# Kernel optimization log

Measured on AMD Instinct MI355X. Metric: run time of the kernel, lower is better.

## Reference

```python
import jax, jax.numpy as jnp
import numpy as np

B, S, D, H, TILES = 4, 1024, 1024, 16, 8
DFF = 4 * D
EPS = 1e-5

def setup_inputs() -> dict:
    key = jax.random.key(0)
    ks = jax.random.split(key, 8)
    p = lambda k, shape: jax.random.normal(k, shape, dtype=jnp.float32) * 0.02
    return dict(
        x=jax.random.normal(ks[0], (B, S, D), dtype=jnp.float32),
        ln1_g=jnp.ones((D,), jnp.float32), ln1_b=jnp.zeros((D,), jnp.float32),
        qkv_w=p(ks[1], (3 * D, D)), qkv_b=jnp.zeros((3 * D,), jnp.float32),
        out_w=p(ks[2], (D, D)), out_b=jnp.zeros((D,), jnp.float32),
        ln2_g=jnp.ones((D,), jnp.float32), ln2_b=jnp.zeros((D,), jnp.float32),
        gate_w=p(ks[3], (TILES, D)), gate_b=jnp.zeros((TILES,), jnp.float32),
        up_W=p(ks[4], (TILES, D, DFF)), up_b=jnp.zeros((TILES, DFF), jnp.float32),
        down_W=p(ks[5], (TILES, DFF, D)), down_b=jnp.zeros((TILES, D), jnp.float32),
    )

def _layernorm(x, g, b):
    m = jnp.mean(x, axis=-1, keepdims=True)
    v = jnp.var(x, axis=-1, keepdims=True)
    return (x - m) * jax.lax.rsqrt(v + EPS) * g + b

def _mha(x, qkv_w, qkv_b, out_w, out_b):
    b, s, d = x.shape
    hd = d // H
    qkv = x @ qkv_w.T + qkv_b                       # [b, s, 3d]
    q, k, v = jnp.split(qkv, 3, axis=-1)
    q = q.reshape(b, s, H, hd)
    k = k.reshape(b, s, H, hd)
    v = v.reshape(b, s, H, hd)
    scores = jnp.einsum('bqhd,bkhd->bhqk', q, k) / jnp.sqrt(jnp.float32(hd))
    p = jax.nn.softmax(scores, axis=-1)
    o = jnp.einsum('bhqk,bkhd->bqhd', p, v).reshape(b, s, d)
    return o @ out_w.T + out_b

def _gated_ffn(t, gate_w, gate_b, up_W, up_b, down_W, down_b):
    # t: [N, D] tokens. Top-1 hard gate with straight-through estimator.
    logits = t @ gate_w.T + gate_b                  # [N, TILES]
    hard = jax.nn.one_hot(jnp.argmax(logits, axis=-1), TILES, dtype=logits.dtype)
    gate = hard + logits - jax.lax.stop_gradient(logits)
    # TriXLinear: one-hot-selected per-tile GEMM, expressed as gated contraction.
    h = jax.nn.relu(jnp.einsum('nt,ni,tio->no', gate, t, up_W) + gate @ up_b)
    out = jnp.einsum('nt,nh,tho->no', gate, h, down_W) + gate @ down_b
    return out, gate

def reference(x, ln1_g, ln1_b, qkv_w, qkv_b, out_w, out_b, ln2_g, ln2_b,
              gate_w, gate_b, up_W, up_b, down_W, down_b):
    n1 = _layernorm(x, ln1_g, ln1_b)
    x = x + _mha(n1, qkv_w, qkv_b, out_w, out_b)
    n2 = _layernorm(x, ln2_g, ln2_b)
    t = n2.reshape(-1, D)
    ffn, gate = _gated_ffn(t, gate_w, gate_b, up_W, up_b, down_W, down_b)
    out = x + ffn.reshape(x.shape)
    return (out, gate.reshape(B, S, TILES))
```

## Files before the change

### kernel.cpp

```cpp
#include <hip/hip_runtime.h>

typedef __attribute__((ext_vector_type(8))) short short8;
typedef __attribute__((ext_vector_type(4))) float f32x4;

__device__ __forceinline__ float bf2f(unsigned short h){
  return __uint_as_float(((unsigned)h) << 16);
}
__device__ __forceinline__ unsigned short f2bf(float f){
  unsigned u = __float_as_uint(f);
  u += 0x7FFFu + ((u >> 16) & 1u);
  return (unsigned short)(u >> 16);
}
__device__ __forceinline__ f32x4 mfma16(short8 a, short8 b, f32x4 c){
  return __builtin_amdgcn_mfma_f32_16x16x32_bf16(a, b, c, 0, 0, 0);
}
__device__ __forceinline__ short8 ld8(const unsigned short* p){
  return *reinterpret_cast<const short8*>(p);
}

__global__ __launch_bounds__(256) void wsplit_k(const float* __restrict__ w,
    unsigned short* __restrict__ hi, unsigned short* __restrict__ lo, int n)
{
  const int i = (blockIdx.x*256 + threadIdx.x)*4;
  if (i >= n) return;
  const float4 v = *(const float4*)(w + i);
  float a[4] = {v.x, v.y, v.z, v.w};
  #pragma unroll
  for (int j=0;j<4;j++){
    unsigned short h = f2bf(a[j]);
    hi[i+j] = h;
    lo[i+j] = f2bf(a[j] - bf2f(h));
  }
}

__global__ __launch_bounds__(256) void wtrans_k(const float* __restrict__ in,
    unsigned short* __restrict__ out, int K, int N)
{
  __shared__ float t[32][33];
  const int z = blockIdx.z;
  const float* inz = in + (long)z*K*N;
  unsigned short* outz = out + (long)z*K*N;
  const int c0 = blockIdx.x*32, r0 = blockIdx.y*32;
  const int tx = threadIdx.x & 31, ty = threadIdx.x >> 5;
  #pragma unroll
  for (int i=0;i<4;i++)
    t[ty+8*i][tx] = inz[(long)(r0+ty+8*i)*N + c0+tx];
  __syncthreads();
  #pragma unroll
  for (int i=0;i<4;i++)
    outz[(long)(c0+ty+8*i)*K + r0+tx] = f2bf(t[tx][ty+8*i]);
}

__global__ __launch_bounds__(256) void ln_k(const float* __restrict__ xin,
    const float* __restrict__ g, const float* __restrict__ bb,
    unsigned short* __restrict__ oh, unsigned short* __restrict__ ol,
    float* __restrict__ ofull)
{
  const int row = blockIdx.x, tid = threadIdx.x;
  const int ln = tid & 63, wv = tid >> 6;
  const float4 f = *(const float4*)(xin + (long)row*1024 + tid*4);
  float v[4] = {f.x, f.y, f.z, f.w};
  float s = v[0]+v[1]+v[2]+v[3];
  float q = v[0]*v[0]+v[1]*v[1]+v[2]*v[2]+v[3]*v[3];
  #pragma unroll
  for (int m=1;m<64;m<<=1){ s += __shfl_xor(s,m,64); q += __shfl_xor(q,m,64); }
  __shared__ float rs[4], rq[4];
  if (ln==0){ rs[wv]=s; rq[wv]=q; }
  __syncthreads();
  s = rs[0]+rs[1]+rs[2]+rs[3];
  q = rq[0]+rq[1]+rq[2]+rq[3];
  const float mean = s * (1.f/1024.f);
  const float var  = q * (1.f/1024.f) - mean*mean;
  const float rinv = 1.f / sqrtf(var + 1e-5f);
  #pragma unroll
  for (int j=0;j<4;j++){
    const int c = tid*4 + j;
    const float nv = (v[j]-mean)*rinv*g[c] + bb[c];
    const unsigned short hi = f2bf(nv);
    oh[(long)row*1024 + c] = hi;
    if (ol)    ol[(long)row*1024 + c] = f2bf(nv - bf2f(hi));
    if (ofull) ofull[(long)row*1024 + c] = nv;
  }
}

template<int AMODE, int EPI, bool GATHER>
__global__ __launch_bounds__(256) void gemm_k(
    const unsigned short* __restrict__ Ah, const unsigned short* __restrict__ Al, int lda,
    const unsigned short* __restrict__ Bh, const unsigned short* __restrict__ Bl,
    int ldb, int K, int N,
    const float* __restrict__ bias,
    const float* __restrict__ resx, const float* __restrict__ resx2,
    unsigned short* __restrict__ oh, unsigned short* __restrict__ ol,
    float* __restrict__ of,
    unsigned short* __restrict__ vt1, unsigned short* __restrict__ vt2,
    const int* __restrict__ idx, const int* __restrict__ cnt, int Mtot)
{
  constexpr int NB = (AMODE==1) ? 2 : 1;
  constexpr int LDW = 40;
  __shared__ unsigned short As[NB][128*LDW];
  __shared__ unsigned short Bs[NB][128*LDW];
  __shared__ long arowS[128];
  __shared__ int  atokS[128];

  const int tid = threadIdx.x, wv = tid>>6, ln = tid&63, l16 = ln&15, qd = ln>>4;
  int M = Mtot;
  int z, mblk, nblk;
  if constexpr (GATHER){
    z = blockIdx.y; mblk = blockIdx.z; nblk = blockIdx.x;
  } else {
    z = blockIdx.z; mblk = blockIdx.x; nblk = blockIdx.y;
  }
  const int* idz = nullptr;
  if constexpr (GATHER){
    M = cnt[z];
    if (mblk*128 >= M) return;
    idz = idx + z*4096;
  }
  const int m0 = mblk*128, n0 = nblk*128;
  const unsigned short* Bz = Bh + (GATHER ? (long)z*(long)K*(long)N : 0);

  if (tid < 128){
    const int mi = m0 + tid;
    const int mc = mi < M ? mi : (M-1);
    const int tok = GATHER ? idz[mc] : mc;
    arowS[tid] = (long)tok * lda;
    atokS[tid] = tok;
  }
  __syncthreads();

  f32x4 acc[4][4];
  #pragma unroll
  for (int i=0;i<4;i++)
    #pragma unroll
    for (int w=0;w<4;w++) acc[i][w] = f32x4{0.f,0.f,0.f,0.f};

  const int mloc = (wv&1)*64, nloc = (wv>>1)*64;
  const int srow0 = tid>>2, scoff = (tid&3)*8;

  for (int k0=0; k0<K; k0+=32){
    #pragma unroll
    for (int i=0;i<2;i++){
      const int row = srow0 + i*64;
      const long ao = arowS[row] + k0 + scoff;
      const long bo = (long)(n0+row)*ldb + k0 + scoff;
      *(short8*)&As[0][row*LDW + scoff] = ld8(Ah + ao);
      *(short8*)&Bs[0][row*LDW + scoff] = ld8(Bz + bo);
      if constexpr (AMODE==1){
        *(short8*)&As[1][row*LDW + scoff] = ld8(Al + ao);
        *(short8*)&Bs[1][row*LDW + scoff] = ld8(Bl + bo);
      }
    }
    __syncthreads();
    short8 a0[4], a1[4], b0[4], b1[4];
    #pragma unroll
    for (int i=0;i<4;i++){
      a0[i] = *(const short8*)&As[0][(mloc+i*16+l16)*LDW + qd*8];
      if constexpr (AMODE==1) a1[i] = *(const short8*)&As[1][(mloc+i*16+l16)*LDW + qd*8];
    }
    #pragma unroll
    for (int w=0;w<4;w++){
      b0[w] = *(const short8*)&Bs[0][(nloc+w*16+l16)*LDW + qd*8];
      if constexpr (AMODE==1) b1[w] = *(const short8*)&Bs[1][(nloc+w*16+l16)*LDW + qd*8];
    }
    #pragma unroll
    for (int i=0;i<4;i++)
      #pragma unroll
      for (int w=0;w<4;w++){
        acc[i][w] = mfma16(a0[i], b0[w], acc[i][w]);
        if constexpr (AMODE==1){
          acc[i][w] = mfma16(a0[i], b1[w], acc[i][w]);
          acc[i][w] = mfma16(a1[i], b0[w], acc[i][w]);
        }
      }
    __syncthreads();
  }
  #pragma unroll
  for (int i=0;i<4;i++){
    #pragma unroll
    for (int w=0;w<4;w++){
      const int col = n0 + nloc + w*16 + l16;
      const float bv = bias[(GATHER ? z*N : 0) + col];
      #pragma unroll
      for (int r=0;r<4;r++){
        const int lrow = mloc + i*16 + qd*4 + r;
        if (m0 + lrow >= M) continue;
        const int tok = atokS[lrow];
        float v = acc[i][w][r] + bv;
        if constexpr (EPI==0){
          const unsigned short hi = f2bf(v);
          const unsigned short lo = f2bf(v - bf2f(hi));
          const long o = (long)tok*3072 + col;
          oh[o] = hi; ol[o] = lo;
          if (col >= 2048){
            const int c = col - 2048;
            const int hh = c >> 6, d = c & 63;
            const int b_ = tok >> 10, ss = tok & 1023;
            const long vo = ((long)((b_*16 + hh)*64 + d))*1024 + ss;
            vt1[vo] = hi; vt2[vo] = lo;
          }
        } else if constexpr (EPI==1){
          v += resx[(long)tok*1024 + col];
          of[(long)tok*1024 + col] = v;
        } else if constexpr (EPI==2){
          v = fmaxf(v, 0.f);
          oh[(long)tok*4096 + col] = f2bf(v);
        } else {
          v += resx2[(long)tok*1024 + col];
          of[(long)tok*1024 + col] = v;
        }
      }
    }
  }
}

__global__ __launch_bounds__(64) void attn_k(
    unsigned short* __restrict__ qkh, unsigned short* __restrict__ qkl,
    const unsigned short* __restrict__ vth, const unsigned short* __restrict__ vtl)
{
  __shared__ float Ps[16][34];
  const int ln = threadIdx.x, l16 = ln&15, qd = ln>>4;
  const int qt = blockIdx.x, h = blockIdx.y, b = blockIdx.z;
  const long qrow = (long)(b*1024 + qt*16 + l16);
  const unsigned short* qp  = qkh + qrow*3072 + h*64 + qd*8;
  const unsigned short* qpl = qkl + qrow*3072 + h*64 + qd*8;
  short8 qh[2], ql[2];
  qh[0] = ld8(qp);  qh[1] = ld8(qp+32);
  ql[0] = ld8(qpl); ql[1] = ld8(qpl+32);
  f32x4 O[4];
  #pragma unroll
  for (int nt=0;nt<4;nt++) O[nt] = f32x4{0.f,0.f,0.f,0.f};
  float mrow[4] = {-3e38f,-3e38f,-3e38f,-3e38f};
  float lrow[4] = {0.f,0.f,0.f,0.f};
  const long vbase = (long)((b*16+h)*64);

  for (int kt=0; kt<32; kt++){
    const int ks0 = kt*32;
    short8 kfh[2][2], kfl[2][2];
    #pragma unroll
    for (int nt2=0;nt2<2;nt2++){
      const long krow = (long)(b*1024 + ks0 + nt2*16 + l16);
      const unsigned short* kp  = qkh + krow*3072 + 1024 + h*64 + qd*8;
      const unsigned short* kpl = qkl + krow*3072 + 1024 + h*64 + qd*8;
      kfh[nt2][0] = ld8(kp);  kfh[nt2][1] = ld8(kp+32);
      kfl[nt2][0] = ld8(kpl); kfl[nt2][1] = ld8(kpl+32);
    }
    f32x4 S0 = f32x4{0.f,0.f,0.f,0.f}, S1 = f32x4{0.f,0.f,0.f,0.f};
    #pragma unroll
    for (int ks=0; ks<2; ks++){
      S0 = mfma16(qh[ks], kfh[0][ks], S0);
      S0 = mfma16(qh[ks], kfl[0][ks], S0);
      S0 = mfma16(ql[ks], kfh[0][ks], S0);
      S1 = mfma16(qh[ks], kfh[1][ks], S1);
      S1 = mfma16(qh[ks], kfl[1][ks], S1);
      S1 = mfma16(ql[ks], kfh[1][ks], S1);
    }
    float p0[4], p1[4], alpha[4];
    #pragma unroll
    for (int r=0;r<4;r++){
      float s0 = S0[r]*0.125f, s1 = S1[r]*0.125f;
      float mx = fmaxf(s0,s1);
      #pragma unroll
      for (int m=1;m<16;m<<=1) mx = fmaxf(mx, __shfl_xor(mx, m, 64));
      float mn = fmaxf(mrow[r], mx);
      float e0 = __expf(s0-mn), e1 = __expf(s1-mn);
      float rsum = e0+e1;
      #pragma unroll
      for (int m=1;m<16;m<<=1) rsum += __shfl_xor(rsum, m, 64);
      float al = __expf(mrow[r]-mn);
      lrow[r] = lrow[r]*al + rsum;
      mrow[r] = mn;
      alpha[r]=al; p0[r]=e0; p1[r]=e1;
    }
    #pragma unroll
    for (int nt=0;nt<4;nt++)
      #pragma unroll
      for (int r=0;r<4;r++) O[nt][r] *= alpha[r];
    #pragma unroll
    for (int r=0;r<4;r++){
      Ps[qd*4+r][l16]      = p0[r];
      Ps[qd*4+r][16+l16]   = p1[r];
    }
    __syncthreads();
    short8 ph, pm, pl;
    #pragma unroll
    for (int j=0;j<8;j++){
      float pv = Ps[l16][qd*8+j];
      unsigned short h1 = f2bf(pv); float r1 = pv - bf2f(h1);
      unsigned short h2 = f2bf(r1); float r2 = r1 - bf2f(h2);
      unsigned short h3 = f2bf(r2);
      ph[j]=(short)h1; pm[j]=(short)h2; pl[j]=(short)h3;
    }
    __syncthreads();
    #pragma unroll
    for (int nt=0;nt<4;nt++){
      const unsigned short* vp  = vth + (vbase + nt*16 + l16)*1024 + ks0 + qd*8;
      const unsigned short* vpl = vtl + (vbase + nt*16 + l16)*1024 + ks0 + qd*8;
      short8 vh = ld8(vp), vl = ld8(vpl);
      O[nt] = mfma16(ph, vh, O[nt]);
      O[nt] = mfma16(ph, vl, O[nt]);
      O[nt] = mfma16(pm, vh, O[nt]);
      O[nt] = mfma16(pl, vh, O[nt]);
    }
  }
  #pragma unroll
  for (int nt=0;nt<4;nt++)
    #pragma unroll
    for (int r=0;r<4;r++){
      float v = O[nt][r] / lrow[r];
      const long row = (long)(b*1024 + qt*16 + qd*4 + r);
      const int col = h*64 + nt*16 + l16;
      const unsigned short hi = f2bf(v);
      qkh[row*3072 + col] = hi;
      qkl[row*3072 + col] = f2bf(v - bf2f(hi));
    }
}

__global__ __launch_bounds__(256) void gate_k(
    const float* __restrict__ n2f, const float* __restrict__ gw, const float* __restrict__ gb,
    float* __restrict__ gout, int* __restrict__ cnt, int* __restrict__ idx)
{
  const int wv = threadIdx.x >> 6, ln = threadIdx.x & 63;
  const int tok = blockIdx.x*4 + wv;
  float xv[16];
  #pragma unroll
  for (int j=0;j<4;j++){
    const float4 f = *(const float4*)(n2f + (long)tok*1024 + ln*16 + j*4);
    xv[j*4]=f.x; xv[j*4+1]=f.y; xv[j*4+2]=f.z; xv[j*4+3]=f.w;
  }
  float lg[8];
  #pragma unroll
  for (int t=0;t<8;t++){
    float s = 0.f;
    #pragma unroll
    for (int j=0;j<4;j++){
      const float4 wf = *(const float4*)(gw + t*1024 + ln*16 + j*4);
      s += xv[j*4]*wf.x + xv[j*4+1]*wf.y + xv[j*4+2]*wf.z + xv[j*4+3]*wf.w;
    }
    #pragma unroll
    for (int m=1;m<64;m<<=1) s += __shfl_xor(s,m,64);
    lg[t] = s + gb[t];
  }
  int best = 0; float bv = lg[0];
  #pragma unroll
  for (int t=1;t<8;t++) if (lg[t] > bv){ bv = lg[t]; best = t; }
  if (ln == 0){
    int pos = atomicAdd(&cnt[best], 1);
    idx[best*4096 + pos] = tok;
  }
  if (ln < 8) gout[(long)tok*8 + ln] = (ln == best) ? 1.0f : 0.0f;
}

extern "C" void kernel_launch(void* const* d_in, const int* in_sizes, int n_in,
                              void* d_out, int out_size, void* d_ws, size_t ws_size,
                              hipStream_t stream)
{
  const float* x     = (const float*)d_in[0];
  const float* ln1g  = (const float*)d_in[1];
  const float* ln1b  = (const float*)d_in[2];
  const float* qkvw  = (const float*)d_in[3];
  const float* qkvb  = (const float*)d_in[4];
  const float* outw  = (const float*)d_in[5];
  const float* outb  = (const float*)d_in[6];
  const float* ln2g  = (const float*)d_in[7];
  const float* ln2b  = (const float*)d_in[8];
  const float* gatew = (const float*)d_in[9];
  const float* gateb = (const float*)d_in[10];
  const float* upW   = (const float*)d_in[11];
  const float* upb   = (const float*)d_in[12];
  const float* dnW   = (const float*)d_in[13];
  const float* dnb   = (const float*)d_in[14];
  float* outp  = (float*)d_out;
  float* gatep = outp + 4194304;

  char* w = (char*)d_ws;
  auto alloc = [&](size_t b){ char* p = w; w += (b + 255) & ~(size_t)255; return p; };
  char* regionA = w;
  unsigned short* n1h  = (unsigned short*)alloc(8388608);
  unsigned short* n1l  = (unsigned short*)alloc(8388608);
  unsigned short* qwh  = (unsigned short*)alloc(6291456);
  unsigned short* qwl  = (unsigned short*)alloc(6291456);
  unsigned short* owh  = (unsigned short*)alloc(2097152);
  unsigned short* owl  = (unsigned short*)alloc(2097152);
  unsigned short* hbuf = (unsigned short*)regionA;
  char* regionB = w;
  unsigned short* qkh  = (unsigned short*)alloc(25165824);
  unsigned short* qkl  = (unsigned short*)alloc(25165824);
  unsigned short* vth  = (unsigned short*)alloc(8388608);
  unsigned short* vtl  = (unsigned short*)alloc(8388608);
  unsigned short* wffn = (unsigned short*)regionB;
  float*          x2   = (float*)alloc(16777216);
  float*          n2f  = (float*)alloc(16777216);
  unsigned short* n2h  = (unsigned short*)alloc(8388608);
  int*            idxb = (int*)alloc(131072);
  int*            cntb = (int*)alloc(256);

  wsplit_k<<<3072,256,0,stream>>>(qkvw, qwh, qwl, 3145728);
  wsplit_k<<<1024,256,0,stream>>>(outw, owh, owl, 1048576);
  ln_k<<<4096,256,0,stream>>>(x, ln1g, ln1b, n1h, n1l, nullptr);
  gemm_k<1,0,false><<<dim3(32,24,1),256,0,stream>>>(
      n1h, n1l, 1024, qwh, qwl, 1024, 1024, 3072, qkvb,
      nullptr, nullptr, qkh, qkl, nullptr, vth, vtl, nullptr, nullptr, 4096);
  attn_k<<<dim3(64,16,4),64,0,stream>>>(qkh, qkl, vth, vtl);
  gemm_k<1,1,false><<<dim3(32,8,1),256,0,stream>>>(
      qkh, qkl, 3072, owh, owl, 1024, 1024, 1024, outb,
      x, nullptr, nullptr, nullptr, x2, nullptr, nullptr, nullptr, nullptr, 4096);
  ln_k<<<4096,256,0,stream>>>(x2, ln2g, ln2b, n2h, nullptr, n2f);
  hipMemsetAsync(cntb, 0, 32, stream);
  gate_k<<<1024,256,0,stream>>>(n2f, gatew, gateb, gatep, cntb, idxb);
  wtrans_k<<<dim3(128,32,8),256,0,stream>>>(upW, wffn, 1024, 4096);
  gemm_k<0,2,true><<<dim3(32,8,32),256,0,stream>>>(
      n2h, nullptr, 1024, wffn, nullptr, 1024, 1024, 4096, upb,
      nullptr, nullptr, hbuf, nullptr, nullptr, nullptr, nullptr, idxb, cntb, 0);
  wtrans_k<<<dim3(32,128,8),256,0,stream>>>(dnW, wffn, 4096, 1024);
  gemm_k<0,3,true><<<dim3(8,8,32),256,0,stream>>>(
      hbuf, nullptr, 4096, wffn, nullptr, 4096, 4096, 1024, dnb,
      nullptr, x2, nullptr, nullptr, outp, nullptr, nullptr, idxb, cntb, 0);
}
```

Before: 1.019 ms.

## Split attention over two key chunks with a separate log-sum-exp merge kernel

The attention kernel now splits the 1024 keys into two halves handled by separate waves, and packs four query-tile waves into each 256-thread block. Each wave writes unnormalised partial outputs plus its running max and sum to a scratch buffer that aliases x2. A new merge kernel combines the two halves with log-sum-exp rescaling and writes the split bf16 hi/lo output. The aim is more waves in flight to hide the latency of the attention loop. The cost is extra partial-result traffic, an additional launch, and scratch writes that exceed x2's allocation and spill into the following buffers.

Result: slower. 1.156 ms (+13.5%).

```diff
diff --git a/kernel.cpp b/kernel.cpp
--- a/kernel.cpp
+++ b/kernel.cpp
@@ -213,13 +213,15 @@
   }
 }
 
-__global__ __launch_bounds__(64) void attn_k(
-    unsigned short* __restrict__ qkh, unsigned short* __restrict__ qkl,
-    const unsigned short* __restrict__ vth, const unsigned short* __restrict__ vtl)
-{
-  __shared__ float Ps[16][34];
-  const int ln = threadIdx.x, l16 = ln&15, qd = ln>>4;
-  const int qt = blockIdx.x, h = blockIdx.y, b = blockIdx.z;
+__global__ __launch_bounds__(256, 8) void attn_k(
+    const unsigned short* __restrict__ qkh, const unsigned short* __restrict__ qkl,
+    const unsigned short* __restrict__ vth, const unsigned short* __restrict__ vtl,
+    float* __restrict__ pbuf)
+{
+  __shared__ float Ps[4][16][34];
+  const int tid = threadIdx.x, wv = tid>>6, ln = tid&63, l16 = ln&15, qd = ln>>4;
+  const int qt = blockIdx.x*4 + wv, h = blockIdx.y;
+  const int c = blockIdx.z >> 2, b = blockIdx.z & 3;
   const long qrow = (long)(b*1024 + qt*16 + l16);
   const unsigned short* qp  = qkh + qrow*3072 + h*64 + qd*8;
   const unsigned short* qpl = qkl + qrow*3072 + h*64 + qd*8;
@@ -233,7 +235,7 @@
   float lrow[4] = {0.f,0.f,0.f,0.f};
   const long vbase = (long)((b*16+h)*64);
 
-  for (int kt=0; kt<32; kt++){
+  for (int kt=c*16; kt<c*16+16; kt++){
     const int ks0 = kt*32;
     short8 kfh[2][2], kfl[2][2];
     #pragma unroll
@@ -277,14 +279,14 @@
       for (int r=0;r<4;r++) O[nt][r] *= alpha[r];
     #pragma unroll
     for (int r=0;r<4;r++){
-      Ps[qd*4+r][l16]      = p0[r];
-      Ps[qd*4+r][16+l16]   = p1[r];
+      Ps[wv][qd*4+r][l16]      = p0[r];
+      Ps[wv][qd*4+r][16+l16]   = p1[r];
     }
     __syncthreads();
     short8 ph, pm, pl;
     #pragma unroll
     for (int j=0;j<8;j++){
-      float pv = Ps[l16][qd*8+j];
+      float pv = Ps[wv][l16][qd*8+j];
       unsigned short h1 = f2bf(pv); float r1 = pv - bf2f(h1);
       unsigned short h2 = f2bf(r1); float r2 = r1 - bf2f(h2);
       unsigned short h3 = f2bf(r2);
@@ -302,17 +304,43 @@
       O[nt] = mfma16(pl, vh, O[nt]);
     }
   }
+  float* pw = pbuf + ((long)(c*4096 + ((b*16+h)<<6) + qt))*1056;
   #pragma unroll
   for (int nt=0;nt<4;nt++)
     #pragma unroll
+    for (int r=0;r<4;r++)
+      pw[(qd*4+r)*64 + nt*16 + l16] = O[nt][r];
+  if (l16 == 0){
+    #pragma unroll
     for (int r=0;r<4;r++){
-      float v = O[nt][r] / lrow[r];
-      const long row = (long)(b*1024 + qt*16 + qd*4 + r);
-      const int col = h*64 + nt*16 + l16;
-      const unsigned short hi = f2bf(v);
-      qkh[row*3072 + col] = hi;
-      qkl[row*3072 + col] = f2bf(v - bf2f(hi));
-    }
+      pw[1024 + qd*4 + r] = mrow[r];
+      pw[1040 + qd*4 + r] = lrow[r];
+    }
+  }
+}
+
+__global__ __launch_bounds__(256) void amerge_k(const float* __restrict__ pbuf,
+    unsigned short* __restrict__ qkh, unsigned short* __restrict__ qkl)
+{
+  const int wv = threadIdx.x>>6, ln = threadIdx.x&63;
+  const int qt = blockIdx.x*4 + wv, h = blockIdx.y, b = blockIdx.z;
+  const long wid = ((b*16+h)<<6) + qt;
+  const float* p1 = pbuf + wid*1056;
+  const float* p2 = pbuf + (4096 + wid)*1056;
+  #pragma unroll
+  for (int row=0;row<16;row++){
+    const float m1 = p1[1024+row], m2 = p2[1024+row];
+    const float l1 = p1[1040+row], l2 = p2[1040+row];
+    const float m = fmaxf(m1,m2);
+    const float e1 = __expf(m1-m), e2 = __expf(m2-m);
+    const float denom = l1*e1 + l2*e2;
+    const float v = (p1[row*64+ln]*e1 + p2[row*64+ln]*e2) / denom;
+    const long rowg = (long)(b*1024 + qt*16 + row);
+    const int col = h*64 + ln;
+    const unsigned short hi = f2bf(v);
+    qkh[rowg*3072 + col] = hi;
+    qkl[rowg*3072 + col] = f2bf(v - bf2f(hi));
+  }
 }
 
 __global__ __launch_bounds__(256) void gate_k(
@@ -393,6 +421,7 @@
   unsigned short* n2h  = (unsigned short*)alloc(8388608);
   int*            idxb = (int*)alloc(131072);
   int*            cntb = (int*)alloc(256);
+  float*          pbuf = x2;
 
   wsplit_k<<<3072,256,0,stream>>>(qkvw, qwh, qwl, 3145728);
   wsplit_k<<<1024,256,0,stream>>>(outw, owh, owl, 1048576);
@@ -400,7 +429,8 @@
   gemm_k<1,0,false><<<dim3(32,24,1),256,0,stream>>>(
       n1h, n1l, 1024, qwh, qwl, 1024, 1024, 3072, qkvb,
       nullptr, nullptr, qkh, qkl, nullptr, vth, vtl, nullptr, nullptr, 4096);
-  attn_k<<<dim3(64,16,4),64,0,stream>>>(qkh, qkl, vth, vtl);
+  attn_k<<<dim3(16,16,8),256,0,stream>>>(qkh, qkl, vth, vtl, pbuf);
+  amerge_k<<<dim3(16,16,4),256,0,stream>>>(pbuf, qkh, qkl);
   gemm_k<1,1,false><<<dim3(32,8,1),256,0,stream>>>(
       qkh, qkl, 3072, owh, owl, 1024, 1024, 1024, outb,
       x, nullptr, nullptr, nullptr, x2, nullptr, nullptr, nullptr, nullptr, 4096);
```

## Share K/V tiles across four attention waves via LDS staging

Applied to the files above, without the earlier changes.

The attention kernel now runs four waves per block, each handling a different 16-row query tile of the same head. Each iteration, the block cooperatively loads the 32-key K tile (hi/lo) and the V^T tile into shared memory once, and all four waves read their MFMA fragments from it. This cuts redundant global/L2 traffic for K and V by four. In exchange it adds block-wide barriers per key step and more LDS use per block, which may reduce occupancy. The launch grid shrinks to match.

Result: faster. 923.1 us (-9.4%).

```diff
diff --git a/kernel.cpp b/kernel.cpp
--- a/kernel.cpp
+++ b/kernel.cpp
@@ -213,13 +213,17 @@
   }
 }
 
-__global__ __launch_bounds__(64) void attn_k(
+__global__ __launch_bounds__(256) void attn_k(
     unsigned short* __restrict__ qkh, unsigned short* __restrict__ qkl,
     const unsigned short* __restrict__ vth, const unsigned short* __restrict__ vtl)
 {
-  __shared__ float Ps[16][34];
-  const int ln = threadIdx.x, l16 = ln&15, qd = ln>>4;
-  const int qt = blockIdx.x, h = blockIdx.y, b = blockIdx.z;
+  constexpr int KP = 72;
+  constexpr int VP = 40;
+  __shared__ unsigned short Kh[32*KP], Kl[32*KP];
+  __shared__ unsigned short Vh[64*VP], Vl[64*VP];
+  __shared__ float Ps[4][16][34];
+  const int tid = threadIdx.x, wv = tid>>6, ln = tid&63, l16 = ln&15, qd = ln>>4;
+  const int qt = blockIdx.x*4 + wv, h = blockIdx.y, b = blockIdx.z;
   const long qrow = (long)(b*1024 + qt*16 + l16);
   const unsigned short* qp  = qkh + qrow*3072 + h*64 + qd*8;
   const unsigned short* qpl = qkl + qrow*3072 + h*64 + qd*8;
@@ -231,18 +235,31 @@
   for (int nt=0;nt<4;nt++) O[nt] = f32x4{0.f,0.f,0.f,0.f};
   float mrow[4] = {-3e38f,-3e38f,-3e38f,-3e38f};
   float lrow[4] = {0.f,0.f,0.f,0.f};
-  const long vbase = (long)((b*16+h)*64);
+
+  const int krow_s = tid>>3, kc8 = (tid&7)*8;
+  const int vrow_s = tid>>2, vc8 = (tid&3)*8;
+  const long kgbase = (long)(b*1024)*3072 + 1024 + h*64 + kc8;
+  const long vgbase = (long)((b*16+h)*64 + vrow_s)*1024 + vc8;
 
   for (int kt=0; kt<32; kt++){
     const int ks0 = kt*32;
+    {
+      const long ko = kgbase + (long)(ks0 + krow_s)*3072;
+      *(short8*)&Kh[krow_s*KP + kc8] = ld8(qkh + ko);
+      *(short8*)&Kl[krow_s*KP + kc8] = ld8(qkl + ko);
+      const long vo = vgbase + ks0;
+      *(short8*)&Vh[vrow_s*VP + vc8] = ld8(vth + vo);
+      *(short8*)&Vl[vrow_s*VP + vc8] = ld8(vtl + vo);
+    }
+    __syncthreads();
     short8 kfh[2][2], kfl[2][2];
     #pragma unroll
     for (int nt2=0;nt2<2;nt2++){
-      const long krow = (long)(b*1024 + ks0 + nt2*16 + l16);
-      const unsigned short* kp  = qkh + krow*3072 + 1024 + h*64 + qd*8;
-      const unsigned short* kpl = qkl + krow*3072 + 1024 + h*64 + qd*8;
-      kfh[nt2][0] = ld8(kp);  kfh[nt2][1] = ld8(kp+32);
-      kfl[nt2][0] = ld8(kpl); kfl[nt2][1] = ld8(kpl+32);
+      #pragma unroll
+      for (int ks=0;ks<2;ks++){
+        kfh[nt2][ks] = *(const short8*)&Kh[(nt2*16+l16)*KP + ks*32 + qd*8];
+        kfl[nt2][ks] = *(const short8*)&Kl[(nt2*16+l16)*KP + ks*32 + qd*8];
+      }
     }
     f32x4 S0 = f32x4{0.f,0.f,0.f,0.f}, S1 = f32x4{0.f,0.f,0.f,0.f};
     #pragma unroll
@@ -277,30 +294,29 @@
       for (int r=0;r<4;r++) O[nt][r] *= alpha[r];
     #pragma unroll
     for (int r=0;r<4;r++){
-      Ps[qd*4+r][l16]      = p0[r];
-      Ps[qd*4+r][16+l16]   = p1[r];
+      Ps[wv][qd*4+r][l16]      = p0[r];
+      Ps[wv][qd*4+r][16+l16]   = p1[r];
     }
     __syncthreads();
     short8 ph, pm, pl;
     #pragma unroll
     for (int j=0;j<8;j++){
-      float pv = Ps[l16][qd*8+j];
+      float pv = Ps[wv][l16][qd*8+j];
       unsigned short h1 = f2bf(pv); float r1 = pv - bf2f(h1);
       unsigned short h2 = f2bf(r1); float r2 = r1 - bf2f(h2);
       unsigned short h3 = f2bf(r2);
       ph[j]=(short)h1; pm[j]=(short)h2; pl[j]=(short)h3;
     }
-    __syncthreads();
     #pragma unroll
     for (int nt=0;nt<4;nt++){
-      const unsigned short* vp  = vth + (vbase + nt*16 + l16)*1024 + ks0 + qd*8;
-      const unsigned short* vpl = vtl + (vbase + nt*16 + l16)*1024 + ks0 + qd*8;
-      short8 vh = ld8(vp), vl = ld8(vpl);
+      short8 vh = *(const short8*)&Vh[(nt*16+l16)*VP + qd*8];
+      short8 vl = *(const short8*)&Vl[(nt*16+l16)*VP + qd*8];
       O[nt] = mfma16(ph, vh, O[nt]);
       O[nt] = mfma16(ph, vl, O[nt]);
       O[nt] = mfma16(pm, vh, O[nt]);
       O[nt] = mfma16(pl, vh, O[nt]);
     }
+    __syncthreads();
   }
   #pragma unroll
   for (int nt=0;nt<4;nt++)
@@ -400,7 +416,7 @@
   gemm_k<1,0,false><<<dim3(32,24,1),256,0,stream>>>(
       n1h, n1l, 1024, qwh, qwl, 1024, 1024, 3072, qkvb,
       nullptr, nullptr, qkh, qkl, nullptr, vth, vtl, nullptr, nullptr, 4096);
-  attn_k<<<dim3(64,16,4),64,0,stream>>>(qkh, qkl, vth, vtl);
+  attn_k<<<dim3(16,16,4),256,0,stream>>>(qkh, qkl, vth, vtl);
   gemm_k<1,1,false><<<dim3(32,8,1),256,0,stream>>>(
       qkh, qkl, 3072, owh, owl, 1024, 1024, 1024, outb,
       x, nullptr, nullptr, nullptr, x2, nullptr, nullptr, nullptr, nullptr, 4096);
```
